# Optimization experiments

Measured on AMD Instinct MI355X. Metric: run time of the kernel, lower is better.

The kernel has to match this reference:

```python
import jax, jax.numpy as jnp
import numpy as np

N, E, H, P = 50000, 300000, 128, 3
NODE_IN, EDGE_IN, OUT = 15, 7, 3


def _ln(x, g, b, eps=1e-5):
    m = jnp.mean(x, axis=-1, keepdims=True)
    v = jnp.mean((x - m) ** 2, axis=-1, keepdims=True)
    return (x - m) * jax.lax.rsqrt(v + eps) * g + b


def _mlp(x, w1, b1, w2, b2):
    # Linear -> ReLU -> Linear (matches MLP(hidden_dims=(H,)))
    return jnp.maximum(x @ w1 + b1, 0.0) @ w2 + b2


def setup_inputs() -> dict:
    key = jax.random.key(0)
    ks = iter(jax.random.split(key, 64))

    def nrm(shape, s=0.05):
        return jax.random.normal(next(ks), shape, dtype=jnp.float32) * s

    inp = {}
    inp['x'] = nrm((N, NODE_IN), 1.0)
    inp['e'] = nrm((E, EDGE_IN), 1.0)
    inp['edge_index'] = jax.random.randint(next(ks), (2, E), 0, N, dtype=jnp.int32)
    # node encoder
    inp['enc_n_w1'] = nrm((NODE_IN, H)); inp['enc_n_b1'] = jnp.zeros((H,), jnp.float32)
    inp['enc_n_w2'] = nrm((H, H)); inp['enc_n_b2'] = jnp.zeros((H,), jnp.float32)
    inp['enc_n_g'] = jnp.ones((H,), jnp.float32); inp['enc_n_be'] = jnp.zeros((H,), jnp.float32)
    # edge encoder
    inp['enc_e_w1'] = nrm((EDGE_IN, H)); inp['enc_e_b1'] = jnp.zeros((H,), jnp.float32)
    inp['enc_e_w2'] = nrm((H, H)); inp['enc_e_b2'] = jnp.zeros((H,), jnp.float32)
    inp['enc_e_g'] = jnp.ones((H,), jnp.float32); inp['enc_e_be'] = jnp.zeros((H,), jnp.float32)
    # per-processor edge MLP (in = 3H) and node MLP (in = 2H), stacked over P steps
    inp['pe_w1'] = nrm((P, 3 * H, H)); inp['pe_b1'] = jnp.zeros((P, H), jnp.float32)
    inp['pe_w2'] = nrm((P, H, H)); inp['pe_b2'] = jnp.zeros((P, H), jnp.float32)
    inp['pe_g'] = jnp.ones((P, H), jnp.float32); inp['pe_be'] = jnp.zeros((P, H), jnp.float32)
    inp['pn_w1'] = nrm((P, 2 * H, H)); inp['pn_b1'] = jnp.zeros((P, H), jnp.float32)
    inp['pn_w2'] = nrm((P, H, H)); inp['pn_b2'] = jnp.zeros((P, H), jnp.float32)
    inp['pn_g'] = jnp.ones((P, H), jnp.float32); inp['pn_be'] = jnp.zeros((P, H), jnp.float32)
    # node decoder (no layer norm)
    inp['dec_w1'] = nrm((H, H)); inp['dec_b1'] = jnp.zeros((H,), jnp.float32)
    inp['dec_w2'] = nrm((H, OUT)); inp['dec_b2'] = jnp.zeros((OUT,), jnp.float32)
    return inp


def _forward(edge_index, x, e,
             enc_n_w1, enc_n_b1, enc_n_w2, enc_n_b2, enc_n_g, enc_n_be,
             enc_e_w1, enc_e_b1, enc_e_w2, enc_e_b2, enc_e_g, enc_e_be,
             pe_w1, pe_b1, pe_w2, pe_b2, pe_g, pe_be,
             pn_w1, pn_b1, pn_w2, pn_b2, pn_g, pn_be,
             dec_w1, dec_b1, dec_w2, dec_b2):
    row, col = edge_index[0], edge_index[1]  # PyG: x_j = x[row] (source), x_i = x[col] (target)
    xh = _ln(_mlp(x, enc_n_w1, enc_n_b1, enc_n_w2, enc_n_b2), enc_n_g, enc_n_be)
    eh = _ln(_mlp(e, enc_e_w1, enc_e_b1, enc_e_w2, enc_e_b2), enc_e_g, enc_e_be)
    for i in range(P):
        # message: edge_mlp(cat[x_i, x_j, edge_attr]) -> scatter-add onto targets (col)
        msg = _ln(_mlp(jnp.concatenate([xh[col], xh[row], eh], axis=-1),
                       pe_w1[i], pe_b1[i], pe_w2[i], pe_b2[i]), pe_g[i], pe_be[i])
        aggr = jax.ops.segment_sum(msg, col, num_segments=N)  # [N, H]
        new_x = _ln(_mlp(jnp.concatenate([aggr, xh], axis=-1),
                         pn_w1[i], pn_b1[i], pn_w2[i], pn_b2[i]), pn_g[i], pn_be[i]) + xh
        # edge update uses cat[x[row], x[col], e] (note: order differs from message)
        new_e = _ln(_mlp(jnp.concatenate([xh[row], xh[col], eh], axis=-1),
                         pe_w1[i], pe_b1[i], pe_w2[i], pe_b2[i]), pe_g[i], pe_be[i]) + eh
        xh, eh = new_x, new_e
    return jnp.maximum(xh @ dec_w1 + dec_b1, 0.0) @ dec_w2 + dec_b2


def reference(x, e, edge_index,
              enc_n_w1, enc_n_b1, enc_n_w2, enc_n_b2, enc_n_g, enc_n_be,
              enc_e_w1, enc_e_b1, enc_e_w2, enc_e_b2, enc_e_g, enc_e_be,
              pe_w1, pe_b1, pe_w2, pe_b2, pe_g, pe_be,
              pn_w1, pn_b1, pn_w2, pn_b2, pn_g, pn_be,
              dec_w1, dec_b1, dec_w2, dec_b2):
    return _forward(edge_index, x, e,
                    enc_n_w1, enc_n_b1, enc_n_w2, enc_n_b2, enc_n_g, enc_n_be,
                    enc_e_w1, enc_e_b1, enc_e_w2, enc_e_b2, enc_e_g, enc_e_be,
                    pe_w1, pe_b1, pe_w2, pe_b2, pe_g, pe_be,
                    pn_w1, pn_b1, pn_w2, pn_b2, pn_g, pn_be,
                    dec_w1, dec_b1, dec_w2, dec_b2)
```

## Files before the change

kernel.cpp:

```cpp
#include <hip/hip_runtime.h>
#include <stdint.h>
#include <math.h>

#define DEVI __device__ __forceinline__

typedef __attribute__((ext_vector_type(8))) _Float16 f16x8;
typedef __attribute__((ext_vector_type(4))) float f32x4;

#define LO_SCALE 2048.0f
#define LO_INV (1.0f / 2048.0f)
#define LO_INV_D (1.0 / 2048.0)
#define AGG_SCALE_D 4194304.0
#define AGG_INV_D (1.0 / 4194304.0)

DEVI unsigned short f2h(float f) {
  union { _Float16 h; unsigned short u; } v; v.h = (_Float16)f; return v.u;
}
DEVI float h2f(unsigned short u) {
  union { unsigned short u; _Float16 h; } v; v.u = u; return (float)v.h;
}
DEVI unsigned short loPart(float v, unsigned short hi) {
  return f2h((v - h2f(hi)) * LO_SCALE);
}
DEVI f32x4 mfma16(f16x8 a, f16x8 b, f32x4 c) {
  return __builtin_amdgcn_mfma_f32_16x16x32_f16(a, b, c, 0, 0, 0);
}
DEVI void mfma4(f16x8 ah, f16x8 al, f16x8 bh, f16x8 bl,
                f32x4& acc, f32x4& accx, f32x4& accy) {
  acc  = mfma16(ah, bh, acc);
  accx = mfma16(ah, bl, accx);
  accx = mfma16(al, bh, accx);
  accy = mfma16(al, bl, accy);
}
DEVI float combine3(float a, float ax, float ay, float b) {
  return (float)((double)a + ((double)ax + (double)ay * LO_INV_D) * LO_INV_D + (double)b);
}
DEVI int swz(int row, int col) { return row * 128 + (col ^ ((row & 7) << 3)); }

struct KParams {
  const unsigned short* w1h; const unsigned short* w1l;
  const unsigned short* w2h; const unsigned short* w2l;
  const float* b1; const float* b2; const float* g; const float* be;
  const float* srcA;
  const unsigned short* xhi;
  const unsigned short* xlo;
  float* xf;
  float* ef;
  unsigned short* xhi_out; unsigned short* xlo_out;
  const int* rowi; const int* coli;
  int* aggi;
  float* out;
  const float* w2f; const float* b2f;
  int nrows; int kin;
};

struct RepackItem { const float* src; unsigned short* dst; int K; int Kt; };
struct RepackParams { RepackItem it[17]; };

__global__ __launch_bounds__(256) void repack_kernel(RepackParams rp) {
  const RepackItem w = rp.it[blockIdx.y];
  const int f = blockIdx.x;
  if (f >= w.Kt * 8) return;
  const int kt = f >> 3, nt = f & 7;
  const size_t loOff = (size_t)w.Kt * 8 * 512;
  for (int s = threadIdx.x; s < 512; s += 256) {
    int ln = s >> 3, j = s & 7;
    int k = kt * 32 + ((ln >> 4) << 3) + j;
    int c = nt * 16 + (ln & 15);
    float v = (k < w.K) ? w.src[(size_t)k * 128 + c] : 0.f;
    unsigned short hi = f2h(v);
    w.dst[(size_t)f * 512 + s] = hi;
    w.dst[loOff + (size_t)f * 512 + s] = loPart(v, hi);
  }
}

template <int MODE>
__global__ __launch_bounds__((MODE == 2) ? 512 : 256, (MODE == 2) ? 1 : 2)
void gnn_kernel(KParams p) {
  constexpr int NT = (MODE == 2) ? 512 : 256;
  constexpr int PHYS = 8192;
  constexpr int NREG = (MODE == 2 || MODE == 3) ? 2 : 1;
  __shared__ __align__(16) unsigned short stA[NREG * 2 * PHYS];
  __shared__ __align__(16) unsigned short wbuf[(MODE == 2) ? 16384 : 1];
  __shared__ float w2s[(MODE == 4) ? 392 : 1];

  const int tid = threadIdx.x;
  const int lane = tid & 63;
  const int wave = tid >> 6;
  const int w4 = (MODE == 2) ? (wave & 3) : wave;
  const int vrt = (MODE == 2) ? (wave >> 2) : 0;
  const int r0 = blockIdx.x * 64;
  const int l15 = lane & 15;
  const int lg = lane >> 4;

  auto HI = [&](int t) { return stA + 2 * t * PHYS; };
  auto LO = [&](int t) { return stA + (2 * t + 1) * PHYS; };

  if constexpr (MODE == 3) {
    for (int s = tid; s < 1024; s += NT) {
      int row = s >> 4, cc = (s & 15) * 8;
      int n = r0 + row;
      int off = swz(row, cc);
      if (n < p.nrows) {
        const int* ap = p.aggi + (size_t)n * 128 + cc;
        union { unsigned short u[8]; f16x8 v; } th, tl;
#pragma unroll
        for (int j = 0; j < 8; j++) {
          float v = (float)((double)ap[j] * AGG_INV_D);
          th.u[j] = f2h(v); tl.u[j] = loPart(v, th.u[j]);
        }
        *(f16x8*)&HI(0)[off] = th.v; *(f16x8*)&LO(0)[off] = tl.v;
        *(f16x8*)&HI(1)[off] = *(const f16x8*)(p.xhi + (size_t)n * 128 + cc);
        *(f16x8*)&LO(1)[off] = *(const f16x8*)(p.xlo + (size_t)n * 128 + cc);
      } else {
        f16x8 z = {0,0,0,0,0,0,0,0};
        *(f16x8*)&HI(0)[off] = z; *(f16x8*)&LO(0)[off] = z;
        *(f16x8*)&HI(1)[off] = z; *(f16x8*)&LO(1)[off] = z;
      }
    }
  } else if constexpr (MODE == 0 || MODE == 1) {
    for (int s = tid; s < 256; s += NT) {
      int row = s >> 2, cc = (s & 3) * 8;
      int n = r0 + row;
      union { unsigned short u[8]; f16x8 v; } th, tl;
#pragma unroll
      for (int j = 0; j < 8; j++) {
        int k = cc + j;
        float v = (n < p.nrows && k < p.kin) ? p.srcA[(size_t)n * p.kin + k] : 0.f;
        th.u[j] = f2h(v); tl.u[j] = loPart(v, th.u[j]);
      }
      int off = swz(row, cc);
      *(f16x8*)&HI(0)[off] = th.v; *(f16x8*)&LO(0)[off] = tl.v;
    }
  } else if constexpr (MODE == 4) {
    for (int s = tid; s < 1024; s += NT) {
      int row = s >> 4, cc = (s & 15) * 8;
      int n = r0 + row;
      int off = swz(row, cc);
      f16x8 z = {0,0,0,0,0,0,0,0};
      if (n < p.nrows) {
        *(f16x8*)&HI(0)[off] = *(const f16x8*)(p.xhi + (size_t)n * 128 + cc);
        *(f16x8*)&LO(0)[off] = *(const f16x8*)(p.xlo + (size_t)n * 128 + cc);
      } else { *(f16x8*)&HI(0)[off] = z; *(f16x8*)&LO(0)[off] = z; }
    }
    for (int s = tid; s < 387; s += NT) w2s[s] = (s < 384) ? p.w2f[s] : p.b2f[s - 384];
  }
  if constexpr (MODE != 2) __syncthreads();

  constexpr int K1T = (MODE == 2) ? 12 : (MODE == 3) ? 8 : (MODE == 4) ? 4 : 1;
  const f32x4 zz = {0.f, 0.f, 0.f, 0.f};
  f32x4 acc1[8], acc1x[8], acc1y[8];
#pragma unroll
  for (int nt = 0; nt < 8; nt++) { acc1[nt] = zz; acc1x[nt] = zz; acc1y[nt] = zz; }
  const int arow = w4 * 16 + l15;
  const int acol = lg << 3;

  if constexpr (MODE == 2) {
    const int ridx = r0 + arow;
    const int ec = (ridx < p.nrows) ? ridx : 0;
    const int nc = p.coli[ec], nr = p.rowi[ec];
    const unsigned short* aH = p.xhi + (size_t)(vrt ? nr : nc) * 128;
    const unsigned short* aL = p.xlo + (size_t)(vrt ? nr : nc) * 128;
    const unsigned short* bH = p.xhi + (size_t)(vrt ? nc : nr) * 128;
    const unsigned short* bL = p.xlo + (size_t)(vrt ? nc : nr) * 128;
    const float* ep = p.ef + (size_t)ec * 128;
    const int t8 = tid * 8;

    *(f16x8*)&wbuf[t8]        = *(const f16x8*)(p.w1h + t8);
    *(f16x8*)&wbuf[4096 + t8] = *(const f16x8*)(p.w1l + t8);
    __syncthreads();

#pragma unroll
    for (int kt = 0; kt < 12; kt++) {
      const int cur = kt & 1;
      const int nxt = cur ^ 1;
      if (kt < 11) {
        *(f16x8*)&wbuf[nxt * 8192 + t8]        = *(const f16x8*)(p.w1h + (kt + 1) * 4096 + t8);
        *(f16x8*)&wbuf[nxt * 8192 + 4096 + t8] = *(const f16x8*)(p.w1l + (kt + 1) * 4096 + t8);
      } else {
        *(f16x8*)&wbuf[nxt * 8192 + t8]        = *(const f16x8*)(p.w2h + t8);
        *(f16x8*)&wbuf[nxt * 8192 + 4096 + t8] = *(const f16x8*)(p.w2l + t8);
      }
      const int kc = (kt & 3) * 32 + acol;
      f16x8 ah, al;
      if (kt < 4)      { ah = *(const f16x8*)(aH + kc); al = *(const f16x8*)(aL + kc); }
      else if (kt < 8) { ah = *(const f16x8*)(bH + kc); al = *(const f16x8*)(bL + kc); }
      else {
        union { unsigned short u[8]; f16x8 v; } th, tl;
#pragma unroll
        for (int j = 0; j < 8; j++) {
          float v = ep[kc + j];
          th.u[j] = f2h(v); tl.u[j] = loPart(v, th.u[j]);
        }
        ah = th.v; al = tl.v;
      }
#pragma unroll
      for (int nt = 0; nt < 8; nt++) {
        f16x8 bh = *(const f16x8*)&wbuf[cur * 8192 + nt * 512 + lane * 8];
        f16x8 bl = *(const f16x8*)&wbuf[cur * 8192 + 4096 + nt * 512 + lane * 8];
        mfma4(ah, al, bh, bl, acc1[nt], acc1x[nt], acc1y[nt]);
      }
      __syncthreads();
    }
  } else {
#pragma unroll
    for (int kt = 0; kt < K1T; kt++) {
      int t = kt >> 2;
      int so = swz(arow, (kt & 3) * 32 + acol);
      f16x8 ah = *(const f16x8*)&HI(t)[so];
      f16x8 al = *(const f16x8*)&LO(t)[so];
#pragma unroll
      for (int nt = 0; nt < 8; nt++) {
        f16x8 bh = *(const f16x8*)&p.w1h[(size_t)(kt * 8 + nt) * 512 + lane * 8];
        f16x8 bl = *(const f16x8*)&p.w1l[(size_t)(kt * 8 + nt) * 512 + lane * 8];
        mfma4(ah, al, bh, bl, acc1[nt], acc1x[nt], acc1y[nt]);
      }
    }
  }

  float b1c[8];
#pragma unroll
  for (int nt = 0; nt < 8; nt++) b1c[nt] = p.b1[nt * 16 + l15];
#pragma unroll
  for (int nt = 0; nt < 8; nt++) {
#pragma unroll
    for (int r = 0; r < 4; r++) {
      int row = w4 * 16 + (lg << 2) + r;
      int col = nt * 16 + l15;
      int off = swz(row, col);
      float v = combine3(acc1[nt][r], acc1x[nt][r], acc1y[nt][r], b1c[nt]);
      v = v > 0.f ? v : 0.f;
      unsigned short hi = f2h(v);
      HI(vrt)[off] = hi; LO(vrt)[off] = loPart(v, hi);
    }
  }

  if constexpr (MODE != 4) {
    f32x4 acc2[8], acc2x[8], acc2y[8];
#pragma unroll
    for (int nt = 0; nt < 8; nt++) { acc2[nt] = zz; acc2x[nt] = zz; acc2y[nt] = zz; }
#pragma unroll
    for (int kt = 0; kt < 4; kt++) {
      if constexpr (MODE == 2) {
        const int cur = (12 + kt) & 1;
        const int nxt = cur ^ 1;
        const int t8 = tid * 8;
        if (kt < 3) {
          *(f16x8*)&wbuf[nxt * 8192 + t8]        = *(const f16x8*)(p.w2h + (kt + 1) * 4096 + t8);
          *(f16x8*)&wbuf[nxt * 8192 + 4096 + t8] = *(const f16x8*)(p.w2l + (kt + 1) * 4096 + t8);
        }
        int so = swz(arow, kt * 32 + acol);
        f16x8 ah = *(const f16x8*)&HI(vrt)[so];
        f16x8 al = *(const f16x8*)&LO(vrt)[so];
#pragma unroll
        for (int nt = 0; nt < 8; nt++) {
          f16x8 bh = *(const f16x8*)&wbuf[cur * 8192 + nt * 512 + lane * 8];
          f16x8 bl = *(const f16x8*)&wbuf[cur * 8192 + 4096 + nt * 512 + lane * 8];
          mfma4(ah, al, bh, bl, acc2[nt], acc2x[nt], acc2y[nt]);
        }
        if (kt < 3) __syncthreads();
      } else {
        int so = swz(arow, kt * 32 + acol);
        f16x8 ah = *(const f16x8*)&HI(vrt)[so];
        f16x8 al = *(const f16x8*)&LO(vrt)[so];
#pragma unroll
        for (int nt = 0; nt < 8; nt++) {
          f16x8 bh = *(const f16x8*)&p.w2h[(size_t)(kt * 8 + nt) * 512 + lane * 8];
          f16x8 bl = *(const f16x8*)&p.w2l[(size_t)(kt * 8 + nt) * 512 + lane * 8];
          mfma4(ah, al, bh, bl, acc2[nt], acc2x[nt], acc2y[nt]);
        }
      }
    }

    float b2c[8], gc[8], bec[8];
#pragma unroll
    for (int nt = 0; nt < 8; nt++) {
      int c = nt * 16 + l15;
      b2c[nt] = p.b2[c]; gc[nt] = p.g[c]; bec[nt] = p.be[c];
    }
    {
      double sum[4] = {0.0, 0.0, 0.0, 0.0};
#pragma unroll
      for (int nt = 0; nt < 8; nt++)
#pragma unroll
        for (int r = 0; r < 4; r++) {
          acc2[nt][r] = combine3(acc2[nt][r], acc2x[nt][r], acc2y[nt][r], b2c[nt]);
          sum[r] += (double)acc2[nt][r];
        }
#pragma unroll
      for (int r = 0; r < 4; r++) {
#pragma unroll
        for (int m = 1; m < 16; m <<= 1) sum[r] += __shfl_xor(sum[r], m);
        sum[r] *= (1.0 / 128.0);
      }
      double vs[4] = {0.0, 0.0, 0.0, 0.0};
#pragma unroll
      for (int nt = 0; nt < 8; nt++)
#pragma unroll
        for (int r = 0; r < 4; r++) {
          double d = (double)acc2[nt][r] - sum[r];
          vs[r] += d * d;
        }
#pragma unroll
      for (int r = 0; r < 4; r++) {
#pragma unroll
        for (int m = 1; m < 16; m <<= 1) vs[r] += __shfl_xor(vs[r], m);
        vs[r] = 1.0 / sqrt(vs[r] * (1.0 / 128.0) + 1e-5);
      }
#pragma unroll
      for (int nt = 0; nt < 8; nt++)
#pragma unroll
        for (int r = 0; r < 4; r++)
          acc2[nt][r] = (float)(((double)acc2[nt][r] - sum[r]) * vs[r]) * gc[nt] + bec[nt];
    }

    if constexpr (MODE == 2) __syncthreads();

#pragma unroll
    for (int r = 0; r < 4; r++) {
      int idx = r0 + w4 * 16 + (lg << 2) + r;
      if (idx >= p.nrows) continue;
      if constexpr (MODE == 0) {
        float* xr = p.xf + (size_t)idx * 128;
        unsigned short* xh_ = p.xhi_out + (size_t)idx * 128;
        unsigned short* xl_ = p.xlo_out + (size_t)idx * 128;
#pragma unroll
        for (int nt = 0; nt < 8; nt++) {
          int c = nt * 16 + l15; float v = acc2[nt][r];
          xr[c] = v;
          unsigned short hi = f2h(v);
          xh_[c] = hi; xl_[c] = loPart(v, hi);
        }
      } else if constexpr (MODE == 1) {
        float* er = p.ef + (size_t)idx * 128;
#pragma unroll
        for (int nt = 0; nt < 8; nt++) er[nt * 16 + l15] = acc2[nt][r];
      } else if constexpr (MODE == 3) {
        float* xr = p.xf + (size_t)idx * 128;
        unsigned short* xh_ = p.xhi_out + (size_t)idx * 128;
        unsigned short* xl_ = p.xlo_out + (size_t)idx * 128;
#pragma unroll
        for (int nt = 0; nt < 8; nt++) {
          int c = nt * 16 + l15;
          float v = acc2[nt][r] + xr[c];
          xr[c] = v;
          unsigned short hi = f2h(v);
          xh_[c] = hi; xl_[c] = loPart(v, hi);
        }
      } else {
        if (vrt == 0) {
          int tgt = p.coli[idx];
          int* ar = p.aggi + (size_t)tgt * 128;
#pragma unroll
          for (int nt = 0; nt < 8; nt++) {
            int q = __double2int_rn((double)acc2[nt][r] * AGG_SCALE_D);
            atomicAdd(&ar[nt * 16 + l15], q);
          }
        } else {
          float* er = p.ef + (size_t)idx * 128;
#pragma unroll
          for (int nt = 0; nt < 8; nt++) {
            int c = nt * 16 + l15;
            er[c] = acc2[nt][r] + er[c];
          }
        }
      }
    }
  } else {
    __syncthreads();
    if (tid < 192) {
      int row = tid / 3, oc = tid - row * 3;
      int n = r0 + row;
      if (n < p.nrows) {
        double s = (double)w2s[384 + oc];
        for (int k = 0; k < 128; k++) {
          int off = swz(row, k);
          double h = (double)h2f(HI(0)[off]) + (double)h2f(LO(0)[off]) * LO_INV_D;
          s += h * (double)w2s[k * 3 + oc];
        }
        p.out[(size_t)n * 3 + oc] = (float)s;
      }
    }
  }
}

extern "C" void kernel_launch(void* const* d_in, const int* in_sizes, int n_in,
                              void* d_out, int out_size, void* d_ws, size_t ws_size,
                              hipStream_t stream) {
  if (n_in < 31) return;
  const int N = in_sizes[0] / 15;
  const int E = in_sizes[1] / 7;
  const float* x        = (const float*)d_in[0];
  const float* ein      = (const float*)d_in[1];
  const int*   eidx     = (const int*)d_in[2];
  const float* enc_n_w1 = (const float*)d_in[3];
  const float* enc_n_b1 = (const float*)d_in[4];
  const float* enc_n_w2 = (const float*)d_in[5];
  const float* enc_n_b2 = (const float*)d_in[6];
  const float* enc_n_g  = (const float*)d_in[7];
  const float* enc_n_be = (const float*)d_in[8];
  const float* enc_e_w1 = (const float*)d_in[9];
  const float* enc_e_b1 = (const float*)d_in[10];
  const float* enc_e_w2 = (const float*)d_in[11];
  const float* enc_e_b2 = (const float*)d_in[12];
  const float* enc_e_g  = (const float*)d_in[13];
  const float* enc_e_be = (const float*)d_in[14];
  const float* pe_w1    = (const float*)d_in[15];
  const float* pe_b1    = (const float*)d_in[16];
  const float* pe_w2    = (const float*)d_in[17];
  const float* pe_b2    = (const float*)d_in[18];
  const float* pe_g     = (const float*)d_in[19];
  const float* pe_be    = (const float*)d_in[20];
  const float* pn_w1    = (const float*)d_in[21];
  const float* pn_b1    = (const float*)d_in[22];
  const float* pn_w2    = (const float*)d_in[23];
  const float* pn_b2    = (const float*)d_in[24];
  const float* pn_g     = (const float*)d_in[25];
  const float* pn_be    = (const float*)d_in[26];
  const float* dec_w1   = (const float*)d_in[27];
  const float* dec_b1   = (const float*)d_in[28];
  const float* dec_w2   = (const float*)d_in[29];
  const float* dec_b2   = (const float*)d_in[30];

  char* ws = (char*)d_ws;
  size_t off = 0;
  auto carve = [&](size_t bytes) -> void* {
    void* pp = ws + off; off += (bytes + 255) & ~(size_t)255; return pp;
  };
  float* xh            = (float*)carve((size_t)N * 128 * 4);
  unsigned short* xhi  = (unsigned short*)carve((size_t)N * 128 * 2);
  unsigned short* xlo  = (unsigned short*)carve((size_t)N * 128 * 2);
  float* eh            = (float*)carve((size_t)E * 128 * 4);
  int* aggi            = (int*)carve((size_t)N * 128 * 4);

  const int ktab[17] = {15, 128, 7, 128, 384, 384, 384, 128, 128, 128,
                        256, 256, 256, 128, 128, 128, 128};
  unsigned short* pk[17];
  for (int i = 0; i < 17; i++) {
    int kt = (ktab[i] + 31) / 32;
    pk[i] = (unsigned short*)carve((size_t)2 * kt * 8 * 512 * 2);
  }
  if (off > ws_size) return;

  RepackParams rp;
  const float* wsrc[17] = {enc_n_w1, enc_n_w2, enc_e_w1, enc_e_w2,
                           pe_w1, pe_w1 + 384 * 128, pe_w1 + 2 * 384 * 128,
                           pe_w2, pe_w2 + 128 * 128, pe_w2 + 2 * 128 * 128,
                           pn_w1, pn_w1 + 256 * 128, pn_w1 + 2 * 256 * 128,
                           pn_w2, pn_w2 + 128 * 128, pn_w2 + 2 * 128 * 128,
                           dec_w1};
  for (int i = 0; i < 17; i++) {
    rp.it[i].src = wsrc[i]; rp.it[i].dst = pk[i];
    rp.it[i].K = ktab[i]; rp.it[i].Kt = (ktab[i] + 31) / 32;
  }
  repack_kernel<<<dim3(96, 17), 256, 0, stream>>>(rp);

  auto wlo = [&](int i) { return pk[i] + (size_t)((ktab[i] + 31) / 32) * 8 * 512; };
  const int gN = (N + 63) / 64, gE = (E + 63) / 64;

  {
    KParams kp{};
    kp.w1h = pk[0]; kp.w1l = wlo(0); kp.w2h = pk[1]; kp.w2l = wlo(1);
    kp.b1 = enc_n_b1; kp.b2 = enc_n_b2; kp.g = enc_n_g; kp.be = enc_n_be;
    kp.srcA = x; kp.xf = xh; kp.xhi_out = xhi; kp.xlo_out = xlo;
    kp.nrows = N; kp.kin = 15;
    gnn_kernel<0><<<gN, 256, 0, stream>>>(kp);
  }
  {
    KParams kp{};
    kp.w1h = pk[2]; kp.w1l = wlo(2); kp.w2h = pk[3]; kp.w2l = wlo(3);
    kp.b1 = enc_e_b1; kp.b2 = enc_e_b2; kp.g = enc_e_g; kp.be = enc_e_be;
    kp.srcA = ein; kp.ef = eh; kp.nrows = E; kp.kin = 7;
    gnn_kernel<1><<<gE, 256, 0, stream>>>(kp);
  }
  for (int i = 0; i < 3; i++) {
    hipMemsetAsync(aggi, 0, (size_t)N * 128 * 4, stream);
    {
      KParams kp{};
      kp.w1h = pk[4 + i]; kp.w1l = wlo(4 + i);
      kp.w2h = pk[7 + i]; kp.w2l = wlo(7 + i);
      kp.b1 = pe_b1 + i * 128; kp.b2 = pe_b2 + i * 128;
      kp.g = pe_g + i * 128; kp.be = pe_be + i * 128;
      kp.xhi = xhi; kp.xlo = xlo; kp.ef = eh;
      kp.rowi = eidx; kp.coli = eidx + E;
      kp.aggi = aggi; kp.nrows = E;
      gnn_kernel<2><<<gE, 512, 0, stream>>>(kp);
    }
    {
      KParams kp{};
      kp.w1h = pk[10 + i]; kp.w1l = wlo(10 + i);
      kp.w2h = pk[13 + i]; kp.w2l = wlo(13 + i);
      kp.b1 = pn_b1 + i * 128; kp.b2 = pn_b2 + i * 128;
      kp.g = pn_g + i * 128; kp.be = pn_be + i * 128;
      kp.aggi = aggi; kp.xhi = xhi; kp.xlo = xlo;
      kp.xf = xh; kp.xhi_out = xhi; kp.xlo_out = xlo; kp.nrows = N;
      gnn_kernel<3><<<gN, 256, 0, stream>>>(kp);
    }
  }
  {
    KParams kp{};
    kp.w1h = pk[16]; kp.w1l = wlo(16); kp.b1 = dec_b1;
    kp.xhi = xhi; kp.xlo = xlo; kp.w2f = dec_w2; kp.b2f = dec_b2;
    kp.out = (float*)d_out; kp.nrows = N;
    gnn_kernel<4><<<gN, 256, 0, stream>>>(kp);
  }
}
```

Before: 2.060 ms.

## Triple-buffer edge-MLP weight tiles and prefetch all gathered activations upfront

In the fused edge-MLP mode, the weight staging buffer in shared memory grows from two slots to three, and weight tiles are prefetched two steps ahead instead of one. All gathered node features (both endpoints) and the converted edge features are loaded into registers before the K loop, so gather latency is no longer paid inside the MFMA loop. This adds shared memory and a sizeable number of live registers (48 f16x8 vectors), which may reduce occupancy or cause spills under the 512-thread launch bound.

```diff
diff --git a/kernel.cpp b/kernel.cpp
--- a/kernel.cpp
+++ b/kernel.cpp
@@ -81,7 +81,7 @@
   constexpr int PHYS = 8192;
   constexpr int NREG = (MODE == 2 || MODE == 3) ? 2 : 1;
   __shared__ __align__(16) unsigned short stA[NREG * 2 * PHYS];
-  __shared__ __align__(16) unsigned short wbuf[(MODE == 2) ? 16384 : 1];
+  __shared__ __align__(16) unsigned short wbuf[(MODE == 2) ? 24576 : 1];
   __shared__ float w2s[(MODE == 4) ? 392 : 1];
 
   const int tid = threadIdx.x;
@@ -164,36 +164,45 @@
     const unsigned short* bH = p.xhi + (size_t)(vrt ? nc : nr) * 128;
     const unsigned short* bL = p.xlo + (size_t)(vrt ? nc : nr) * 128;
     const float* ep = p.ef + (size_t)ec * 128;
+    f16x8 Ah[4], Al[4], Bh[4], Bl[4], Eh[4], El[4];
+#pragma unroll
+    for (int q = 0; q < 4; q++) {
+      const int kc = q * 32 + acol;
+      Ah[q] = *(const f16x8*)(aH + kc); Al[q] = *(const f16x8*)(aL + kc);
+      Bh[q] = *(const f16x8*)(bH + kc); Bl[q] = *(const f16x8*)(bL + kc);
+    }
+#pragma unroll
+    for (int q = 0; q < 4; q++) {
+      const int kc = q * 32 + acol;
+      union { unsigned short u[8]; f16x8 v; } th, tl;
+#pragma unroll
+      for (int j = 0; j < 8; j++) {
+        float v = ep[kc + j];
+        th.u[j] = f2h(v); tl.u[j] = loPart(v, th.u[j]);
+      }
+      Eh[q] = th.v; El[q] = tl.v;
+    }
+
     const int t8 = tid * 8;
-
-    *(f16x8*)&wbuf[t8]        = *(const f16x8*)(p.w1h + t8);
-    *(f16x8*)&wbuf[4096 + t8] = *(const f16x8*)(p.w1l + t8);
+    auto wsH = [&](int s) { return (s < 12) ? p.w1h + s * 4096 : p.w2h + (s - 12) * 4096; };
+    auto wsL = [&](int s) { return (s < 12) ? p.w1l + s * 4096 : p.w2l + (s - 12) * 4096; };
+    *(f16x8*)&wbuf[t8]               = *(const f16x8*)(wsH(0) + t8);
+    *(f16x8*)&wbuf[4096 + t8]        = *(const f16x8*)(wsL(0) + t8);
+    *(f16x8*)&wbuf[8192 + t8]        = *(const f16x8*)(wsH(1) + t8);
+    *(f16x8*)&wbuf[8192 + 4096 + t8] = *(const f16x8*)(wsL(1) + t8);
     __syncthreads();
 
 #pragma unroll
     for (int kt = 0; kt < 12; kt++) {
-      const int cur = kt & 1;
-      const int nxt = cur ^ 1;
-      if (kt < 11) {
-        *(f16x8*)&wbuf[nxt * 8192 + t8]        = *(const f16x8*)(p.w1h + (kt + 1) * 4096 + t8);
-        *(f16x8*)&wbuf[nxt * 8192 + 4096 + t8] = *(const f16x8*)(p.w1l + (kt + 1) * 4096 + t8);
-      } else {
-        *(f16x8*)&wbuf[nxt * 8192 + t8]        = *(const f16x8*)(p.w2h + t8);
-        *(f16x8*)&wbuf[nxt * 8192 + 4096 + t8] = *(const f16x8*)(p.w2l + t8);
-      }
-      const int kc = (kt & 3) * 32 + acol;
+      const int cur = kt % 3;
+      const int pre = (kt + 2) % 3;
+      *(f16x8*)&wbuf[pre * 8192 + t8]        = *(const f16x8*)(wsH(kt + 2) + t8);
+      *(f16x8*)&wbuf[pre * 8192 + 4096 + t8] = *(const f16x8*)(wsL(kt + 2) + t8);
+      const int q = kt & 3;
       f16x8 ah, al;
-      if (kt < 4)      { ah = *(const f16x8*)(aH + kc); al = *(const f16x8*)(aL + kc); }
-      else if (kt < 8) { ah = *(const f16x8*)(bH + kc); al = *(const f16x8*)(bL + kc); }
-      else {
-        union { unsigned short u[8]; f16x8 v; } th, tl;
-#pragma unroll
-        for (int j = 0; j < 8; j++) {
-          float v = ep[kc + j];
-          th.u[j] = f2h(v); tl.u[j] = loPart(v, th.u[j]);
-        }
-        ah = th.v; al = tl.v;
-      }
+      if (kt < 4)      { ah = Ah[q]; al = Al[q]; }
+      else if (kt < 8) { ah = Bh[q]; al = Bl[q]; }
+      else             { ah = Eh[q]; al = El[q]; }
 #pragma unroll
       for (int nt = 0; nt < 8; nt++) {
         f16x8 bh = *(const f16x8*)&wbuf[cur * 8192 + nt * 512 + lane * 8];
@@ -242,12 +251,12 @@
 #pragma unroll
     for (int kt = 0; kt < 4; kt++) {
       if constexpr (MODE == 2) {
-        const int cur = (12 + kt) & 1;
-        const int nxt = cur ^ 1;
+        const int cur = (12 + kt) % 3;
+        const int pre = (14 + kt) % 3;
         const int t8 = tid * 8;
-        if (kt < 3) {
-          *(f16x8*)&wbuf[nxt * 8192 + t8]        = *(const f16x8*)(p.w2h + (kt + 1) * 4096 + t8);
-          *(f16x8*)&wbuf[nxt * 8192 + 4096 + t8] = *(const f16x8*)(p.w2l + (kt + 1) * 4096 + t8);
+        if (kt < 2) {
+          *(f16x8*)&wbuf[pre * 8192 + t8]        = *(const f16x8*)(p.w2h + (kt + 2) * 4096 + t8);
+          *(f16x8*)&wbuf[pre * 8192 + 4096 + t8] = *(const f16x8*)(p.w2l + (kt + 2) * 4096 + t8);
         }
         int so = swz(arow, kt * 32 + acol);
         f16x8 ah = *(const f16x8*)&HI(vrt)[so];
```

Result: slower. 2.246 ms (+9.0%).

## Stage gathered edge-MLP inputs in shared memory before the K loop

Applied to the files above, without the earlier changes.

In the edge-MLP mode, the kernel now gathers the x[col], x[row] and edge-feature rows for the 64-edge tile into swizzled LDS with coalesced 16-byte loads up front, instead of each lane loading its A fragments from global memory inside the K loop. The two wave groups (message and edge-update orderings) then read the same staged tiles with a permuted tile index. This removes the duplicated gathers across the two wave halves and the global-load latency inside the MFMA loop. In exchange, LDS use grows to three hi/lo tile pairs plus the weight buffer, and an extra barrier is added before the loop.

```diff
diff --git a/kernel.cpp b/kernel.cpp
--- a/kernel.cpp
+++ b/kernel.cpp
@@ -79,8 +79,8 @@
 void gnn_kernel(KParams p) {
   constexpr int NT = (MODE == 2) ? 512 : 256;
   constexpr int PHYS = 8192;
-  constexpr int NREG = (MODE == 2 || MODE == 3) ? 2 : 1;
-  __shared__ __align__(16) unsigned short stA[NREG * 2 * PHYS];
+  constexpr int NTILE = (MODE == 2) ? 3 : (MODE == 3 ? 2 : 1);
+  __shared__ __align__(16) unsigned short stA[NTILE * 2 * PHYS];
   __shared__ __align__(16) unsigned short wbuf[(MODE == 2) ? 16384 : 1];
   __shared__ float w2s[(MODE == 4) ? 392 : 1];
 
@@ -96,7 +96,35 @@
   auto HI = [&](int t) { return stA + 2 * t * PHYS; };
   auto LO = [&](int t) { return stA + (2 * t + 1) * PHYS; };
 
-  if constexpr (MODE == 3) {
+  if constexpr (MODE == 2) {
+    for (int s = tid; s < 1024; s += NT) {
+      int row = s >> 4, cc = (s & 15) * 8;
+      int e = r0 + row;
+      int off = swz(row, cc);
+      if (e < p.nrows) {
+        int nc = p.coli[e], nr = p.rowi[e];
+        *(f16x8*)&HI(0)[off] = *(const f16x8*)(p.xhi + (size_t)nc * 128 + cc);
+        *(f16x8*)&LO(0)[off] = *(const f16x8*)(p.xlo + (size_t)nc * 128 + cc);
+        *(f16x8*)&HI(1)[off] = *(const f16x8*)(p.xhi + (size_t)nr * 128 + cc);
+        *(f16x8*)&LO(1)[off] = *(const f16x8*)(p.xlo + (size_t)nr * 128 + cc);
+        const float* sp = p.ef + (size_t)e * 128 + cc;
+        union { unsigned short u[8]; f16x8 v; } th, tl;
+#pragma unroll
+        for (int j = 0; j < 8; j++) {
+          float v = sp[j];
+          th.u[j] = f2h(v); tl.u[j] = loPart(v, th.u[j]);
+        }
+        *(f16x8*)&HI(2)[off] = th.v; *(f16x8*)&LO(2)[off] = tl.v;
+      } else {
+        f16x8 z = {0,0,0,0,0,0,0,0};
+#pragma unroll
+        for (int t = 0; t < 3; t++) { *(f16x8*)&HI(t)[off] = z; *(f16x8*)&LO(t)[off] = z; }
+      }
+    }
+    const int t8 = tid * 8;
+    *(f16x8*)&wbuf[t8]        = *(const f16x8*)(p.w1h + t8);
+    *(f16x8*)&wbuf[4096 + t8] = *(const f16x8*)(p.w1l + t8);
+  } else if constexpr (MODE == 3) {
     for (int s = tid; s < 1024; s += NT) {
       int row = s >> 4, cc = (s & 15) * 8;
       int n = r0 + row;
@@ -145,7 +173,7 @@
     }
     for (int s = tid; s < 387; s += NT) w2s[s] = (s < 384) ? p.w2f[s] : p.b2f[s - 384];
   }
-  if constexpr (MODE != 2) __syncthreads();
+  __syncthreads();
 
   constexpr int K1T = (MODE == 2) ? 12 : (MODE == 3) ? 8 : (MODE == 4) ? 4 : 1;
   const f32x4 zz = {0.f, 0.f, 0.f, 0.f};
@@ -156,20 +184,7 @@
   const int acol = lg << 3;
 
   if constexpr (MODE == 2) {
-    const int ridx = r0 + arow;
-    const int ec = (ridx < p.nrows) ? ridx : 0;
-    const int nc = p.coli[ec], nr = p.rowi[ec];
-    const unsigned short* aH = p.xhi + (size_t)(vrt ? nr : nc) * 128;
-    const unsigned short* aL = p.xlo + (size_t)(vrt ? nr : nc) * 128;
-    const unsigned short* bH = p.xhi + (size_t)(vrt ? nc : nr) * 128;
-    const unsigned short* bL = p.xlo + (size_t)(vrt ? nc : nr) * 128;
-    const float* ep = p.ef + (size_t)ec * 128;
     const int t8 = tid * 8;
-
-    *(f16x8*)&wbuf[t8]        = *(const f16x8*)(p.w1h + t8);
-    *(f16x8*)&wbuf[4096 + t8] = *(const f16x8*)(p.w1l + t8);
-    __syncthreads();
-
 #pragma unroll
     for (int kt = 0; kt < 12; kt++) {
       const int cur = kt & 1;
@@ -181,19 +196,11 @@
         *(f16x8*)&wbuf[nxt * 8192 + t8]        = *(const f16x8*)(p.w2h + t8);
         *(f16x8*)&wbuf[nxt * 8192 + 4096 + t8] = *(const f16x8*)(p.w2l + t8);
       }
-      const int kc = (kt & 3) * 32 + acol;
-      f16x8 ah, al;
-      if (kt < 4)      { ah = *(const f16x8*)(aH + kc); al = *(const f16x8*)(aL + kc); }
-      else if (kt < 8) { ah = *(const f16x8*)(bH + kc); al = *(const f16x8*)(bL + kc); }
-      else {
-        union { unsigned short u[8]; f16x8 v; } th, tl;
-#pragma unroll
-        for (int j = 0; j < 8; j++) {
-          float v = ep[kc + j];
-          th.u[j] = f2h(v); tl.u[j] = loPart(v, th.u[j]);
-        }
-        ah = th.v; al = tl.v;
-      }
+      const int tM = kt >> 2;
+      const int t = vrt ? ((tM == 0) ? 1 : (tM == 1) ? 0 : 2) : tM;
+      const int so = swz(arow, (kt & 3) * 32 + acol);
+      f16x8 ah = *(const f16x8*)&HI(t)[so];
+      f16x8 al = *(const f16x8*)&LO(t)[so];
 #pragma unroll
       for (int nt = 0; nt < 8; nt++) {
         f16x8 bh = *(const f16x8*)&wbuf[cur * 8192 + nt * 512 + lane * 8];
```

After: 1.954 ms. 1.05x faster.
